# Kernel optimization log

Hardware: AMD Instinct MI355X
Metric: run time of the kernel (lower is better)

The kernel has to match this reference:

```python
import jax, jax.numpy as jnp
import numpy as np

C_IN = 256
C_INT = C_IN // 2  # inter_channels


def _conv1x1(x, w, b):
    # x: [B, Cin, H, W], w: [Cout, Cin], b: [Cout]
    return jnp.einsum('bchw,oc->bohw', x, w) + b[None, :, None, None]


def setup_inputs() -> dict:
    key = jax.random.key(0)
    ks = jax.random.split(key, 9)
    B, H, W = 8, 64, 64
    s_in = 1.0 / np.sqrt(C_IN)
    s_int = 1.0 / np.sqrt(C_INT)
    return {
        'x': jax.random.normal(ks[0], (B, C_IN, H, W), dtype=jnp.float32),
        'g_w': jax.random.normal(ks[1], (C_INT, C_IN), dtype=jnp.float32) * s_in,
        'g_b': jax.random.normal(ks[2], (C_INT,), dtype=jnp.float32) * s_in,
        'theta_w': jax.random.normal(ks[3], (C_INT, C_IN), dtype=jnp.float32) * s_in,
        'theta_b': jax.random.normal(ks[4], (C_INT,), dtype=jnp.float32) * s_in,
        'phi_w': jax.random.normal(ks[5], (C_INT, C_IN), dtype=jnp.float32) * s_in,
        'phi_b': jax.random.normal(ks[6], (C_INT,), dtype=jnp.float32) * s_in,
        'W_w': jax.random.normal(ks[7], (C_IN, C_INT), dtype=jnp.float32) * s_int,
        'W_b': jax.random.normal(ks[8], (C_IN,), dtype=jnp.float32) * s_int,
    }


def reference(x, g_w, g_b, theta_w, theta_b, phi_w, phi_b, W_w, W_b):
    B, C, H, W = x.shape
    N = H * W
    g_x = _conv1x1(x, g_w, g_b).reshape(B, C_INT, N)        # [B, Ci, N]
    theta_x = _conv1x1(x, theta_w, theta_b).reshape(B, C_INT, N)
    phi_x = _conv1x1(x, phi_w, phi_b).reshape(B, C_INT, N)
    # f[b, i, j] = theta[:, i] . phi[:, j]  (no scaling, per original)
    f = jnp.einsum('bci,bcj->bij', theta_x, phi_x)          # [B, N, N]
    f_div_C = jax.nn.softmax(f, axis=-1)
    y = jnp.einsum('bij,bcj->bci', f_div_C, g_x)            # [B, Ci, N]
    y = y.reshape(B, C_INT, H, W)
    y = _conv1x1(y, W_w, W_b)                               # [B, C, H, W]
    return x + y
```

## Files before the change

kernel.cpp:

```cpp
#include <hip/hip_runtime.h>

typedef _Float16 f16;
typedef _Float16 f16x4 __attribute__((ext_vector_type(4)));
typedef _Float16 f16x8 __attribute__((ext_vector_type(8)));
typedef __fp16 h2 __attribute__((ext_vector_type(2)));
typedef float f32x4 __attribute__((ext_vector_type(4)));
typedef float f32x16 __attribute__((ext_vector_type(16)));

#define MFMA16(a, b, c) __builtin_amdgcn_mfma_f32_16x16x32_f16(a, b, c, 0, 0, 0)
#define MFMA32(a, b, c) __builtin_amdgcn_mfma_f32_32x32x16_f16(a, b, c, 0, 0, 0)

#if defined(__has_builtin)
#if __has_builtin(__builtin_amdgcn_fdot2)
#define HAS_FDOT2 1
#endif
#endif

typedef const __attribute__((address_space(1))) void gvoid;
typedef __attribute__((address_space(3))) void lvoid;
#define GLDS16(g, l) __builtin_amdgcn_global_load_lds((gvoid*)(g), (lvoid*)(l), 16, 0, 0)

__global__ __launch_bounds__(256) void wcvt_k(
    const float* __restrict__ tw, const float* __restrict__ pw,
    const float* __restrict__ gw, const float* __restrict__ ww,
    f16* __restrict__ Wall, f16* __restrict__ Wepi) {
  int i = blockIdx.x * 256 + threadIdx.x;
  if (i < 384 * 256) {
    int c = i >> 8, cp = i & 255;
    float v = (c < 128) ? tw[c * 256 + cp]
            : (c < 256) ? pw[(c - 128) * 256 + cp]
                        : gw[(c - 256) * 256 + cp];
    Wall[i] = (f16)v;
  }
  int j = i - 384 * 256;
  if (j >= 0 && j < 256 * 128) Wepi[j] = (f16)ww[j];
}

__global__ __launch_bounds__(256) void proj_k(
    const float* __restrict__ x, const f16* __restrict__ Wall,
    const float* __restrict__ tb, const float* __restrict__ pb,
    const float* __restrict__ gb, f16* __restrict__ Q, f16* __restrict__ K,
    f16* __restrict__ Vt) {
  __shared__ f16 xs[64 * 264];
  __shared__ f16 vs[128 * 65];
  int b = blockIdx.x >> 6, nt = blockIdx.x & 63;
  int nbase = nt * 64;
  int tid = threadIdx.x;

  int nq = tid & 15, kq0 = tid >> 4;
#pragma unroll
  for (int p = 0; p < 4; ++p) {
    int kq = kq0 + 16 * p;
    float4 ld[4];
#pragma unroll
    for (int j = 0; j < 4; ++j)
      ld[j] = *(const float4*)(x + ((size_t)b * 256 + 4 * kq + j) * 4096 + nbase + 4 * nq);
#pragma unroll
    for (int e = 0; e < 4; ++e) {
      f16x4 wv = {(f16)((&ld[0].x)[e]), (f16)((&ld[1].x)[e]), (f16)((&ld[2].x)[e]),
                  (f16)((&ld[3].x)[e])};
      *(f16x4*)(&xs[(4 * nq + e) * 264 + 4 * kq]) = wv;
    }
  }
  __syncthreads();

  int w = tid >> 6, lane = tid & 63;
  int lr = lane & 15, lhi = lane >> 4;
  f16x8 a[8];
#pragma unroll
  for (int ks = 0; ks < 8; ++ks)
    a[ks] = *(const f16x8*)(&xs[(w * 16 + lr) * 264 + ks * 32 + lhi * 8]);
  f32x4 acc[24];
#pragma unroll
  for (int ct = 0; ct < 24; ++ct) {
    acc[ct] = {0.f, 0.f, 0.f, 0.f};
    const f16x8* wr = (const f16x8*)(Wall + (size_t)(ct * 16 + lr) * 256);
#pragma unroll
    for (int ks = 0; ks < 8; ++ks) acc[ct] = MFMA16(a[ks], wr[ks * 4 + lhi], acc[ct]);
  }
  int nloc = w * 16 + lhi * 4;
#pragma unroll
  for (int ct = 0; ct < 24; ++ct) {
    int c = ct * 16 + lr;
    float bias = (c < 128) ? tb[c] : (c < 256) ? pb[c - 128] : gb[c - 256];
#pragma unroll
    for (int r = 0; r < 4; ++r) {
      float v = acc[ct][r] + bias;
      int n = nbase + nloc + r;
      if (c < 128) {
        Q[((size_t)b * 4096 + n) * 128 + c] = (f16)v;
      } else if (c < 256) {
        int d = c - 128;
        int slot = ((d >> 4) << 6) + ((n & 31) << 1) + ((d >> 3) & 1);
        K[(size_t)b * 524288 + (size_t)(n >> 5) * 4096 + slot * 8 + (d & 7)] = (f16)v;
      } else {
        vs[(c - 256) * 65 + nloc + r] = (f16)v;
      }
    }
  }
  __syncthreads();
  f16* vo = Vt + (size_t)b * 524288;
  for (int rep = 0; rep < 32; ++rep) {
    int idx = rep * 256 + tid;
    int c = idx >> 6, j = idx & 63;
    int n = nbase + j;
    int nl = j & 31;
    int p = (nl & 3) | ((nl & 4) << 1) | ((nl & 8) >> 1) | (nl & 16);
    int g = p >> 3, e = p & 7;
    int slot = ((c >> 5) << 7) + ((g >> 1) << 6) + ((c & 31) << 1) + (g & 1);
    vo[(size_t)(n >> 5) * 4096 + slot * 8 + e] = vs[c * 65 + j];
  }
}

__global__ __launch_bounds__(256, 3) void attn_k(const f16* __restrict__ Q,
                                                 const f16* __restrict__ K,
                                                 const f16* __restrict__ Vt,
                                                 f16* __restrict__ Yp,
                                                 float2* __restrict__ ml) {
  __shared__ f16 Ks[2][32 * 128];
  __shared__ f16 Vs[2][128 * 32];
  const float L = 1.44269504f;
  int swzid = ((blockIdx.x & 7) << 7) | ((int)blockIdx.x >> 3);
  int b = swzid >> 7, rem = swzid & 127;
  int qt = rem >> 2, s = rem & 3;
  int qbase = qt * 128;
  int tile0 = s * 32;
  int tid = threadIdx.x;
  int w = tid >> 6, lane = tid & 63;
  int col = lane & 31, hi = lane >> 5;

  const f16* Qr = Q + ((size_t)b * 4096 + qbase + w * 32 + col) * 128;
  f16x8 bq[8];
#pragma unroll
  for (int ks = 0; ks < 8; ++ks) bq[ks] = *(const f16x8*)(Qr + ks * 16 + hi * 8);

  f32x16 yacc[4];
#pragma unroll
  for (int dt = 0; dt < 4; ++dt)
#pragma unroll
    for (int r = 0; r < 16; ++r) yacc[dt][r] = 0.f;
  float lv[4] = {0.f, 0.f, 0.f, 0.f};
  float m = -1e30f, nmL = 1e30f;

  const char* KbB = (const char*)(K + (size_t)b * 524288);
  const char* VbB = (const char*)(Vt + (size_t)b * 524288);
  char* KsB = (char*)&Ks[0][0];
  char* VsB = (char*)&Vs[0][0];

  auto stage = [&](int t, int buf) {
    size_t tb_ = (size_t)(tile0 + t) * 8192;
    const char* kb = KbB + tb_ + w * 2048 + lane * 16;
    const char* vb = VbB + tb_ + w * 2048 + lane * 16;
    char* kl = KsB + buf * 8192 + w * 2048;
    char* vl = VsB + buf * 8192 + w * 2048;
#pragma unroll
    for (int c = 0; c < 2; ++c) {
      GLDS16(kb + c * 1024, kl + c * 1024);
      GLDS16(vb + c * 1024, vl + c * 1024);
    }
  };

  int lanebase = col * 32 + hi * 16;

  stage(0, 0);

  for (int t = 0; t < 32; ++t) {
    int cur = t & 1;
    __syncthreads();
    if (t + 1 < 32) stage(t + 1, cur ^ 1);

    f32x16 s2;
#pragma unroll
    for (int r = 0; r < 16; ++r) s2[r] = 0.f;
    __builtin_amdgcn_s_setprio(1);
    {
      const char* kcur = KsB + cur * 8192 + lanebase;
#pragma unroll
      for (int ks = 0; ks < 8; ++ks) {
        f16x8 ak = *(const f16x8*)(kcur + ks * 1024);
        s2 = MFMA32(ak, bq[ks], s2);
      }
    }
    __builtin_amdgcn_s_setprio(0);

    float a0 = fmaxf(fmaxf(s2[0], s2[1]), s2[2]);
    float a1 = fmaxf(fmaxf(s2[3], s2[4]), s2[5]);
    float a2 = fmaxf(fmaxf(s2[6], s2[7]), s2[8]);
    float a3 = fmaxf(fmaxf(s2[9], s2[10]), s2[11]);
    float a4 = fmaxf(fmaxf(s2[12], s2[13]), s2[14]);
    float pm = fmaxf(fmaxf(fmaxf(a0, a1), fmaxf(a2, a3)), fmaxf(a4, s2[15]));
    pm = fmaxf(pm, __shfl_xor(pm, 32));
    if (pm > m + 8.f) {
      float sc = __expf(m - pm);
      m = pm;
      nmL = -m * L;
#pragma unroll
      for (int i = 0; i < 4; ++i) lv[i] *= sc;
#pragma unroll
      for (int dt = 0; dt < 4; ++dt)
#pragma unroll
        for (int r = 0; r < 16; ++r) yacc[dt][r] *= sc;
    }
#pragma unroll
    for (int r = 0; r < 16; ++r) s2[r] = exp2f(fmaf(s2[r], L, nmL));

    f16x8 pfrA, pfrB;
#pragma unroll
    for (int c = 0; c < 8; ++c) {
      pfrA[c] = (f16)s2[c];
      pfrB[c] = (f16)s2[8 + c];
    }
#if defined(HAS_FDOT2)
    {
      h2 one2 = {1.0f, 1.0f};
      const h2* pa = (const h2*)&pfrA;
      const h2* pb2 = (const h2*)&pfrB;
#pragma unroll
      for (int j = 0; j < 4; ++j) {
        lv[j] = __builtin_amdgcn_fdot2(pa[j], one2, lv[j], false);
        lv[j] = __builtin_amdgcn_fdot2(pb2[j], one2, lv[j], false);
      }
    }
#else
#pragma unroll
    for (int j = 0; j < 4; ++j)
      lv[j] += (float)pfrA[2 * j] + (float)pfrA[2 * j + 1] + (float)pfrB[2 * j] +
               (float)pfrB[2 * j + 1];
#endif

    __builtin_amdgcn_s_setprio(1);
    {
      const char* vcur = VsB + cur * 8192 + lanebase;
#pragma unroll
      for (int dt = 0; dt < 4; ++dt) {
        f16x8 av0 = *(const f16x8*)(vcur + dt * 2048);
        yacc[dt] = MFMA32(av0, pfrA, yacc[dt]);
        f16x8 av1 = *(const f16x8*)(vcur + dt * 2048 + 1024);
        yacc[dt] = MFMA32(av1, pfrB, yacc[dt]);
      }
    }
    __builtin_amdgcn_s_setprio(0);
  }

  float l = (lv[0] + lv[1]) + (lv[2] + lv[3]);
  l += __shfl_xor(l, 32);

  int rowG = b * 4096 + qbase + w * 32 + col;
  f16* yo = Yp + ((size_t)s * 32768 + rowG) * 128;
  float inv = 1.0f / l;
#pragma unroll
  for (int dt = 0; dt < 4; ++dt)
#pragma unroll
    for (int a = 0; a < 4; ++a) {
      f16x4 ov = {(f16)(yacc[dt][4 * a] * inv), (f16)(yacc[dt][4 * a + 1] * inv),
                  (f16)(yacc[dt][4 * a + 2] * inv), (f16)(yacc[dt][4 * a + 3] * inv)};
      *(f16x4*)(yo + dt * 32 + a * 8 + hi * 4) = ov;
    }
  if (hi == 0) ml[s * 32768 + rowG] = make_float2(m, l);
}

__global__ __launch_bounds__(256) void epi_k(const f16* __restrict__ Yp,
                                             const float2* __restrict__ ml,
                                             const f16* __restrict__ Wepi,
                                             const float* __restrict__ Wb,
                                             const float* __restrict__ x,
                                             float* __restrict__ out) {
  int b = blockIdx.x >> 6, nt = blockIdx.x & 63;
  int nbase = nt * 64;
  int w = threadIdx.x >> 6, lane = threadIdx.x & 63;
  int lr = lane & 15, lhi = lane >> 4;
  f16x8 by[4][4];
#pragma unroll
  for (int n4 = 0; n4 < 4; ++n4) {
    int row = b * 4096 + nbase + n4 * 16 + lr;
    float2 m0 = ml[row], m1 = ml[32768 + row], m2 = ml[65536 + row], m3 = ml[98304 + row];
    float mm = fmaxf(fmaxf(m0.x, m1.x), fmaxf(m2.x, m3.x));
    float w0 = m0.y * __expf(m0.x - mm), w1 = m1.y * __expf(m1.x - mm);
    float w2 = m2.y * __expf(m2.x - mm), w3 = m3.y * __expf(m3.x - mm);
    float inv = 1.f / (w0 + w1 + w2 + w3);
    w0 *= inv; w1 *= inv; w2 *= inv; w3 *= inv;
    size_t rb = (size_t)row * 128;
#pragma unroll
    for (int ks = 0; ks < 4; ++ks) {
      int eo = ks * 32 + lhi * 8;
      f16x8 a0 = *(const f16x8*)(Yp + rb + eo);
      f16x8 a1 = *(const f16x8*)(Yp + (size_t)32768 * 128 + rb + eo);
      f16x8 a2 = *(const f16x8*)(Yp + (size_t)65536 * 128 + rb + eo);
      f16x8 a3 = *(const f16x8*)(Yp + (size_t)98304 * 128 + rb + eo);
      f16x8 o;
#pragma unroll
      for (int e = 0; e < 8; ++e)
        o[e] = (f16)(w0 * (float)a0[e] + w1 * (float)a1[e] + w2 * (float)a2[e] +
                     w3 * (float)a3[e]);
      by[n4][ks] = o;
    }
  }
#pragma unroll
  for (int ot = 0; ot < 4; ++ot) {
    int o0 = w * 64 + ot * 16;
    const f16x8* wr = (const f16x8*)(Wepi + (size_t)(o0 + lr) * 128);
    f16x8 a[4];
#pragma unroll
    for (int ks = 0; ks < 4; ++ks) a[ks] = wr[ks * 4 + lhi];
#pragma unroll
    for (int n4 = 0; n4 < 4; ++n4) {
      f32x4 acc = {0.f, 0.f, 0.f, 0.f};
#pragma unroll
      for (int ks = 0; ks < 4; ++ks) acc = MFMA16(a[ks], by[n4][ks], acc);
#pragma unroll
      for (int r = 0; r < 4; ++r) {
        int o = o0 + lhi * 4 + r;
        int n = nbase + n4 * 16 + lr;
        size_t idx = ((size_t)b * 256 + o) * 4096 + n;
        out[idx] = x[idx] + Wb[o] + acc[r];
      }
    }
  }
}

extern "C" void kernel_launch(void* const* d_in, const int* in_sizes, int n_in,
                              void* d_out, int out_size, void* d_ws, size_t ws_size,
                              hipStream_t stream) {
  const float* x       = (const float*)d_in[0];
  const float* g_w     = (const float*)d_in[1];
  const float* g_b     = (const float*)d_in[2];
  const float* theta_w = (const float*)d_in[3];
  const float* theta_b = (const float*)d_in[4];
  const float* phi_w   = (const float*)d_in[5];
  const float* phi_b   = (const float*)d_in[6];
  const float* W_w     = (const float*)d_in[7];
  const float* W_b     = (const float*)d_in[8];
  float* out = (float*)d_out;

  f16* Q    = (f16*)d_ws;
  f16* Kk   = Q + (size_t)8 * 4096 * 128;
  f16* Vt   = Kk + (size_t)8 * 4096 * 128;
  f16* Wall = Vt + (size_t)8 * 4096 * 128;
  f16* Wepi = Wall + 384 * 256;
  float2* ml = (float2*)(Wepi + 256 * 128);
  f16* Yp   = (f16*)(ml + 4 * 32768);

  wcvt_k<<<512, 256, 0, stream>>>(theta_w, phi_w, g_w, W_w, Wall, Wepi);
  proj_k<<<512, 256, 0, stream>>>(x, Wall, theta_b, phi_b, g_b, Q, Kk, Vt);
  attn_k<<<1024, 256, 0, stream>>>(Q, Kk, Vt, Yp, ml);
  epi_k<<<512, 256, 0, stream>>>(Yp, ml, Wepi, W_b, x, out);
}
```

Measured before the change: 190.5 us.

## Double attention block to 512 threads sharing K/V tiles across 256 queries

```diff
diff --git a/kernel.cpp b/kernel.cpp
--- a/kernel.cpp
+++ b/kernel.cpp
@@ -112,7 +112,7 @@
   }
 }
 
-__global__ __launch_bounds__(256, 3) void attn_k(const f16* __restrict__ Q,
+__global__ __launch_bounds__(512, 4) void attn_k(const f16* __restrict__ Q,
                                                  const f16* __restrict__ K,
                                                  const f16* __restrict__ Vt,
                                                  f16* __restrict__ Yp,
@@ -120,10 +120,10 @@
   __shared__ f16 Ks[2][32 * 128];
   __shared__ f16 Vs[2][128 * 32];
   const float L = 1.44269504f;
-  int swzid = ((blockIdx.x & 7) << 7) | ((int)blockIdx.x >> 3);
-  int b = swzid >> 7, rem = swzid & 127;
+  int b = blockIdx.x & 7;
+  int rem = (int)blockIdx.x >> 3;
   int qt = rem >> 2, s = rem & 3;
-  int qbase = qt * 128;
+  int qbase = qt * 256;
   int tile0 = s * 32;
   int tid = threadIdx.x;
   int w = tid >> 6, lane = tid & 63;
@@ -139,7 +139,7 @@
   for (int dt = 0; dt < 4; ++dt)
 #pragma unroll
     for (int r = 0; r < 16; ++r) yacc[dt][r] = 0.f;
-  float lv[4] = {0.f, 0.f, 0.f, 0.f};
+  float lv[2] = {0.f, 0.f};
   float m = -1e30f, nmL = 1e30f;
 
   const char* KbB = (const char*)(K + (size_t)b * 524288);
@@ -148,16 +148,9 @@
   char* VsB = (char*)&Vs[0][0];
 
   auto stage = [&](int t, int buf) {
-    size_t tb_ = (size_t)(tile0 + t) * 8192;
-    const char* kb = KbB + tb_ + w * 2048 + lane * 16;
-    const char* vb = VbB + tb_ + w * 2048 + lane * 16;
-    char* kl = KsB + buf * 8192 + w * 2048;
-    char* vl = VsB + buf * 8192 + w * 2048;
-#pragma unroll
-    for (int c = 0; c < 2; ++c) {
-      GLDS16(kb + c * 1024, kl + c * 1024);
-      GLDS16(vb + c * 1024, vl + c * 1024);
-    }
+    size_t tb_ = (size_t)(tile0 + t) * 8192 + tid * 16;
+    GLDS16(KbB + tb_, KsB + buf * 8192 + tid * 16);
+    GLDS16(VbB + tb_, VsB + buf * 8192 + tid * 16);
   };
 
   int lanebase = col * 32 + hi * 16;
@@ -194,8 +187,8 @@
       float sc = __expf(m - pm);
       m = pm;
       nmL = -m * L;
-#pragma unroll
-      for (int i = 0; i < 4; ++i) lv[i] *= sc;
+      lv[0] *= sc;
+      lv[1] *= sc;
 #pragma unroll
       for (int dt = 0; dt < 4; ++dt)
 #pragma unroll
@@ -217,15 +210,16 @@
       const h2* pb2 = (const h2*)&pfrB;
 #pragma unroll
       for (int j = 0; j < 4; ++j) {
-        lv[j] = __builtin_amdgcn_fdot2(pa[j], one2, lv[j], false);
-        lv[j] = __builtin_amdgcn_fdot2(pb2[j], one2, lv[j], false);
+        lv[0] = __builtin_amdgcn_fdot2(pa[j], one2, lv[0], false);
+        lv[1] = __builtin_amdgcn_fdot2(pb2[j], one2, lv[1], false);
       }
     }
 #else
 #pragma unroll
-    for (int j = 0; j < 4; ++j)
-      lv[j] += (float)pfrA[2 * j] + (float)pfrA[2 * j + 1] + (float)pfrB[2 * j] +
-               (float)pfrB[2 * j + 1];
+    for (int j = 0; j < 4; ++j) {
+      lv[0] += (float)pfrA[2 * j] + (float)pfrA[2 * j + 1];
+      lv[1] += (float)pfrB[2 * j] + (float)pfrB[2 * j + 1];
+    }
 #endif
 
     __builtin_amdgcn_s_setprio(1);
@@ -242,7 +236,7 @@
     __builtin_amdgcn_s_setprio(0);
   }
 
-  float l = (lv[0] + lv[1]) + (lv[2] + lv[3]);
+  float l = lv[0] + lv[1];
   l += __shfl_xor(l, 32);
 
   int rowG = b * 4096 + qbase + w * 32 + col;
@@ -342,6 +336,6 @@
 
   wcvt_k<<<512, 256, 0, stream>>>(theta_w, phi_w, g_w, W_w, Wall, Wepi);
   proj_k<<<512, 256, 0, stream>>>(x, Wall, theta_b, phi_b, g_b, Q, Kk, Vt);
-  attn_k<<<1024, 256, 0, stream>>>(Q, Kk, Vt, Yp, ml);
+  attn_k<<<512, 512, 0, stream>>>(Q, Kk, Vt, Yp, ml);
   epi_k<<<512, 256, 0, stream>>>(Yp, ml, Wepi, W_b, x, out);
 }
```

Measured after the change: 193.4 us. No clear change (+1.5%).

## Software-pipeline attention with 4-stage LDS ring and halve KV split count

Applied to the files above, without the earlier changes.

```diff
diff --git a/kernel.cpp b/kernel.cpp
--- a/kernel.cpp
+++ b/kernel.cpp
@@ -112,19 +112,19 @@
   }
 }
 
-__global__ __launch_bounds__(256, 3) void attn_k(const f16* __restrict__ Q,
+__global__ __launch_bounds__(256, 2) void attn_k(const f16* __restrict__ Q,
                                                  const f16* __restrict__ K,
                                                  const f16* __restrict__ Vt,
                                                  f16* __restrict__ Yp,
                                                  float2* __restrict__ ml) {
-  __shared__ f16 Ks[2][32 * 128];
-  __shared__ f16 Vs[2][128 * 32];
+  __shared__ f16 Ks[4][32 * 128];
+  __shared__ f16 Vs[4][128 * 32];
   const float L = 1.44269504f;
-  int swzid = ((blockIdx.x & 7) << 7) | ((int)blockIdx.x >> 3);
-  int b = swzid >> 7, rem = swzid & 127;
-  int qt = rem >> 2, s = rem & 3;
+  int swzid = ((blockIdx.x & 7) << 6) | ((int)blockIdx.x >> 3);
+  int b = swzid >> 6, rem = swzid & 63;
+  int qt = rem >> 1, s = rem & 1;
   int qbase = qt * 128;
-  int tile0 = s * 32;
+  int tile0 = s * 64;
   int tid = threadIdx.x;
   int w = tid >> 6, lane = tid & 63;
   int col = lane & 31, hi = lane >> 5;
@@ -147,12 +147,12 @@
   char* KsB = (char*)&Ks[0][0];
   char* VsB = (char*)&Vs[0][0];
 
-  auto stage = [&](int t, int buf) {
+  auto stage = [&](int t) {
     size_t tb_ = (size_t)(tile0 + t) * 8192;
     const char* kb = KbB + tb_ + w * 2048 + lane * 16;
     const char* vb = VbB + tb_ + w * 2048 + lane * 16;
-    char* kl = KsB + buf * 8192 + w * 2048;
-    char* vl = VsB + buf * 8192 + w * 2048;
+    char* kl = KsB + (t & 3) * 8192 + w * 2048;
+    char* vl = VsB + (t & 3) * 8192 + w * 2048;
 #pragma unroll
     for (int c = 0; c < 2; ++c) {
       GLDS16(kb + c * 1024, kl + c * 1024);
@@ -162,33 +162,26 @@
 
   int lanebase = col * 32 + hi * 16;
 
-  stage(0, 0);
-
-  for (int t = 0; t < 32; ++t) {
-    int cur = t & 1;
-    __syncthreads();
-    if (t + 1 < 32) stage(t + 1, cur ^ 1);
-
-    f32x16 s2;
-#pragma unroll
-    for (int r = 0; r < 16; ++r) s2[r] = 0.f;
+  auto qkt = [&](int p, f32x16& sN) {
+    const char* kcur = KsB + (p & 3) * 8192 + lanebase;
+#pragma unroll
+    for (int r = 0; r < 16; ++r) sN[r] = 0.f;
     __builtin_amdgcn_s_setprio(1);
-    {
-      const char* kcur = KsB + cur * 8192 + lanebase;
-#pragma unroll
-      for (int ks = 0; ks < 8; ++ks) {
-        f16x8 ak = *(const f16x8*)(kcur + ks * 1024);
-        s2 = MFMA32(ak, bq[ks], s2);
-      }
+#pragma unroll
+    for (int ks = 0; ks < 8; ++ks) {
+      f16x8 ak = *(const f16x8*)(kcur + ks * 1024);
+      sN = MFMA32(ak, bq[ks], sN);
     }
     __builtin_amdgcn_s_setprio(0);
-
-    float a0 = fmaxf(fmaxf(s2[0], s2[1]), s2[2]);
-    float a1 = fmaxf(fmaxf(s2[3], s2[4]), s2[5]);
-    float a2 = fmaxf(fmaxf(s2[6], s2[7]), s2[8]);
-    float a3 = fmaxf(fmaxf(s2[9], s2[10]), s2[11]);
-    float a4 = fmaxf(fmaxf(s2[12], s2[13]), s2[14]);
-    float pm = fmaxf(fmaxf(fmaxf(a0, a1), fmaxf(a2, a3)), fmaxf(a4, s2[15]));
+  };
+
+  auto smpv = [&](int t, f32x16& sO) {
+    float a0 = fmaxf(fmaxf(sO[0], sO[1]), sO[2]);
+    float a1 = fmaxf(fmaxf(sO[3], sO[4]), sO[5]);
+    float a2 = fmaxf(fmaxf(sO[6], sO[7]), sO[8]);
+    float a3 = fmaxf(fmaxf(sO[9], sO[10]), sO[11]);
+    float a4 = fmaxf(fmaxf(sO[12], sO[13]), sO[14]);
+    float pm = fmaxf(fmaxf(fmaxf(a0, a1), fmaxf(a2, a3)), fmaxf(a4, sO[15]));
     pm = fmaxf(pm, __shfl_xor(pm, 32));
     if (pm > m + 8.f) {
       float sc = __expf(m - pm);
@@ -202,13 +195,13 @@
         for (int r = 0; r < 16; ++r) yacc[dt][r] *= sc;
     }
 #pragma unroll
-    for (int r = 0; r < 16; ++r) s2[r] = exp2f(fmaf(s2[r], L, nmL));
+    for (int r = 0; r < 16; ++r) sO[r] = exp2f(fmaf(sO[r], L, nmL));
 
     f16x8 pfrA, pfrB;
 #pragma unroll
     for (int c = 0; c < 8; ++c) {
-      pfrA[c] = (f16)s2[c];
-      pfrB[c] = (f16)s2[8 + c];
+      pfrA[c] = (f16)sO[c];
+      pfrB[c] = (f16)sO[8 + c];
     }
 #if defined(HAS_FDOT2)
     {
@@ -227,20 +220,54 @@
       lv[j] += (float)pfrA[2 * j] + (float)pfrA[2 * j + 1] + (float)pfrB[2 * j] +
                (float)pfrB[2 * j + 1];
 #endif
-
     __builtin_amdgcn_s_setprio(1);
-    {
-      const char* vcur = VsB + cur * 8192 + lanebase;
-#pragma unroll
-      for (int dt = 0; dt < 4; ++dt) {
-        f16x8 av0 = *(const f16x8*)(vcur + dt * 2048);
-        yacc[dt] = MFMA32(av0, pfrA, yacc[dt]);
-        f16x8 av1 = *(const f16x8*)(vcur + dt * 2048 + 1024);
-        yacc[dt] = MFMA32(av1, pfrB, yacc[dt]);
-      }
+    const char* vcur = VsB + (t & 3) * 8192 + lanebase;
+#pragma unroll
+    for (int dt = 0; dt < 4; ++dt) {
+      f16x8 av0 = *(const f16x8*)(vcur + dt * 2048);
+      yacc[dt] = MFMA32(av0, pfrA, yacc[dt]);
+      f16x8 av1 = *(const f16x8*)(vcur + dt * 2048 + 1024);
+      yacc[dt] = MFMA32(av1, pfrB, yacc[dt]);
     }
     __builtin_amdgcn_s_setprio(0);
-  }
+  };
+
+#define PH_WAIT4 asm volatile("s_waitcnt vmcnt(4)" ::: "memory")
+#define PH_WAIT0 asm volatile("s_waitcnt vmcnt(0)" ::: "memory")
+
+  f32x16 sA, sB;
+  stage(0);
+  stage(1);
+  PH_WAIT4;
+  __builtin_amdgcn_s_barrier();
+  stage(2);
+  qkt(0, sA);
+  PH_WAIT4;
+  __builtin_amdgcn_s_barrier();
+  stage(3);
+  qkt(1, sB);
+  smpv(0, sA);
+  for (int p = 2; p < 62; p += 2) {
+    PH_WAIT4;
+    __builtin_amdgcn_s_barrier();
+    stage(p + 2);
+    qkt(p, sA);
+    smpv(p - 1, sB);
+    PH_WAIT4;
+    __builtin_amdgcn_s_barrier();
+    stage(p + 3);
+    qkt(p + 1, sB);
+    smpv(p, sA);
+  }
+  PH_WAIT4;
+  __builtin_amdgcn_s_barrier();
+  qkt(62, sA);
+  smpv(61, sB);
+  PH_WAIT0;
+  __builtin_amdgcn_s_barrier();
+  qkt(63, sB);
+  smpv(62, sA);
+  smpv(63, sB);
 
   float l = (lv[0] + lv[1]) + (lv[2] + lv[3]);
   l += __shfl_xor(l, 32);
@@ -269,29 +296,26 @@
   int nbase = nt * 64;
   int w = threadIdx.x >> 6, lane = threadIdx.x & 63;
   int lr = lane & 15, lhi = lane >> 4;
+  const f16* yb1 = Yp + (size_t)32768 * 128;
   f16x8 by[4][4];
 #pragma unroll
   for (int n4 = 0; n4 < 4; ++n4) {
     int row = b * 4096 + nbase + n4 * 16 + lr;
-    float2 m0 = ml[row], m1 = ml[32768 + row], m2 = ml[65536 + row], m3 = ml[98304 + row];
-    float mm = fmaxf(fmaxf(m0.x, m1.x), fmaxf(m2.x, m3.x));
+    float2 m0 = ml[row], m1 = ml[32768 + row];
+    float mm = fmaxf(m0.x, m1.x);
     float w0 = m0.y * __expf(m0.x - mm), w1 = m1.y * __expf(m1.x - mm);
-    float w2 = m2.y * __expf(m2.x - mm), w3 = m3.y * __expf(m3.x - mm);
-    float inv = 1.f / (w0 + w1 + w2 + w3);
-    w0 *= inv; w1 *= inv; w2 *= inv; w3 *= inv;
+    float inv = 1.f / (w0 + w1);
+    w0 *= inv;
+    w1 *= inv;
     size_t rb = (size_t)row * 128;
 #pragma unroll
     for (int ks = 0; ks < 4; ++ks) {
       int eo = ks * 32 + lhi * 8;
       f16x8 a0 = *(const f16x8*)(Yp + rb + eo);
-      f16x8 a1 = *(const f16x8*)(Yp + (size_t)32768 * 128 + rb + eo);
-      f16x8 a2 = *(const f16x8*)(Yp + (size_t)65536 * 128 + rb + eo);
-      f16x8 a3 = *(const f16x8*)(Yp + (size_t)98304 * 128 + rb + eo);
+      f16x8 a1 = *(const f16x8*)(yb1 + rb + eo);
       f16x8 o;
 #pragma unroll
-      for (int e = 0; e < 8; ++e)
-        o[e] = (f16)(w0 * (float)a0[e] + w1 * (float)a1[e] + w2 * (float)a2[e] +
-                     w3 * (float)a3[e]);
+      for (int e = 0; e < 8; ++e) o[e] = (f16)(w0 * (float)a0[e] + w1 * (float)a1[e]);
       by[n4][ks] = o;
     }
   }
@@ -338,10 +362,10 @@
   f16* Wall = Vt + (size_t)8 * 4096 * 128;
   f16* Wepi = Wall + 384 * 256;
   float2* ml = (float2*)(Wepi + 256 * 128);
-  f16* Yp   = (f16*)(ml + 4 * 32768);
+  f16* Yp   = (f16*)(ml + 2 * 32768);
 
   wcvt_k<<<512, 256, 0, stream>>>(theta_w, phi_w, g_w, W_w, Wall, Wepi);
   proj_k<<<512, 256, 0, stream>>>(x, Wall, theta_b, phi_b, g_b, Q, Kk, Vt);
-  attn_k<<<1024, 256, 0, stream>>>(Q, Kk, Vt, Yp, ml);
+  attn_k<<<512, 256, 0, stream>>>(Q, Kk, Vt, Yp, ml);
   epi_k<<<512, 256, 0, stream>>>(Yp, ml, Wepi, W_b, x, out);
 }
```

After: 184.8 us, median of 2. 3.0% less time.

## Process two 32-row query tiles per wave in attention kernel to reuse K/V loads

Applied to the files above, without the earlier changes.

```diff
diff --git a/kernel.cpp b/kernel.cpp
--- a/kernel.cpp
+++ b/kernel.cpp
@@ -112,7 +112,7 @@
   }
 }
 
-__global__ __launch_bounds__(256, 3) void attn_k(const f16* __restrict__ Q,
+__global__ __launch_bounds__(256, 2) void attn_k(const f16* __restrict__ Q,
                                                  const f16* __restrict__ K,
                                                  const f16* __restrict__ Vt,
                                                  f16* __restrict__ Yp,
@@ -120,27 +120,34 @@
   __shared__ f16 Ks[2][32 * 128];
   __shared__ f16 Vs[2][128 * 32];
   const float L = 1.44269504f;
-  int swzid = ((blockIdx.x & 7) << 7) | ((int)blockIdx.x >> 3);
-  int b = swzid >> 7, rem = swzid & 127;
+  int swzid = ((blockIdx.x & 7) << 6) | ((int)blockIdx.x >> 3);
+  int b = swzid >> 6, rem = swzid & 63;
   int qt = rem >> 2, s = rem & 3;
-  int qbase = qt * 128;
+  int qbase = qt * 256;
   int tile0 = s * 32;
   int tid = threadIdx.x;
   int w = tid >> 6, lane = tid & 63;
   int col = lane & 31, hi = lane >> 5;
 
-  const f16* Qr = Q + ((size_t)b * 4096 + qbase + w * 32 + col) * 128;
-  f16x8 bq[8];
-#pragma unroll
-  for (int ks = 0; ks < 8; ++ks) bq[ks] = *(const f16x8*)(Qr + ks * 16 + hi * 8);
-
-  f32x16 yacc[4];
+  const f16* Qr = Q + ((size_t)b * 4096 + qbase + w * 64 + col) * 128;
+  f16x8 bq0[8], bq1[8];
+#pragma unroll
+  for (int ks = 0; ks < 8; ++ks) {
+    bq0[ks] = *(const f16x8*)(Qr + ks * 16 + hi * 8);
+    bq1[ks] = *(const f16x8*)(Qr + 32 * 128 + ks * 16 + hi * 8);
+  }
+
+  f32x16 y0[4], y1[4];
 #pragma unroll
   for (int dt = 0; dt < 4; ++dt)
 #pragma unroll
-    for (int r = 0; r < 16; ++r) yacc[dt][r] = 0.f;
-  float lv[4] = {0.f, 0.f, 0.f, 0.f};
-  float m = -1e30f, nmL = 1e30f;
+    for (int r = 0; r < 16; ++r) {
+      y0[dt][r] = 0.f;
+      y1[dt][r] = 0.f;
+    }
+  float lv0 = 0.f, lv1 = 0.f;
+  float m0 = -1e30f, nmL0 = 1e30f;
+  float m1 = -1e30f, nmL1 = 1e30f;
 
   const char* KbB = (const char*)(K + (size_t)b * 524288);
   const char* VbB = (const char*)(Vt + (size_t)b * 524288);
@@ -169,63 +176,106 @@
     __syncthreads();
     if (t + 1 < 32) stage(t + 1, cur ^ 1);
 
-    f32x16 s2;
-#pragma unroll
-    for (int r = 0; r < 16; ++r) s2[r] = 0.f;
+    f32x16 s0, s1;
+#pragma unroll
+    for (int r = 0; r < 16; ++r) {
+      s0[r] = 0.f;
+      s1[r] = 0.f;
+    }
     __builtin_amdgcn_s_setprio(1);
     {
       const char* kcur = KsB + cur * 8192 + lanebase;
 #pragma unroll
       for (int ks = 0; ks < 8; ++ks) {
         f16x8 ak = *(const f16x8*)(kcur + ks * 1024);
-        s2 = MFMA32(ak, bq[ks], s2);
+        s0 = MFMA32(ak, bq0[ks], s0);
+        s1 = MFMA32(ak, bq1[ks], s1);
       }
     }
     __builtin_amdgcn_s_setprio(0);
 
-    float a0 = fmaxf(fmaxf(s2[0], s2[1]), s2[2]);
-    float a1 = fmaxf(fmaxf(s2[3], s2[4]), s2[5]);
-    float a2 = fmaxf(fmaxf(s2[6], s2[7]), s2[8]);
-    float a3 = fmaxf(fmaxf(s2[9], s2[10]), s2[11]);
-    float a4 = fmaxf(fmaxf(s2[12], s2[13]), s2[14]);
-    float pm = fmaxf(fmaxf(fmaxf(a0, a1), fmaxf(a2, a3)), fmaxf(a4, s2[15]));
-    pm = fmaxf(pm, __shfl_xor(pm, 32));
-    if (pm > m + 8.f) {
-      float sc = __expf(m - pm);
-      m = pm;
-      nmL = -m * L;
-#pragma unroll
-      for (int i = 0; i < 4; ++i) lv[i] *= sc;
-#pragma unroll
-      for (int dt = 0; dt < 4; ++dt)
-#pragma unroll
-        for (int r = 0; r < 16; ++r) yacc[dt][r] *= sc;
-    }
-#pragma unroll
-    for (int r = 0; r < 16; ++r) s2[r] = exp2f(fmaf(s2[r], L, nmL));
-
-    f16x8 pfrA, pfrB;
-#pragma unroll
-    for (int c = 0; c < 8; ++c) {
-      pfrA[c] = (f16)s2[c];
-      pfrB[c] = (f16)s2[8 + c];
+    f16x8 p0A, p0B, p1A, p1B;
+    {
+      float a0 = fmaxf(fmaxf(s0[0], s0[1]), s0[2]);
+      float a1 = fmaxf(fmaxf(s0[3], s0[4]), s0[5]);
+      float a2 = fmaxf(fmaxf(s0[6], s0[7]), s0[8]);
+      float a3 = fmaxf(fmaxf(s0[9], s0[10]), s0[11]);
+      float a4 = fmaxf(fmaxf(s0[12], s0[13]), s0[14]);
+      float pm = fmaxf(fmaxf(fmaxf(a0, a1), fmaxf(a2, a3)), fmaxf(a4, s0[15]));
+      pm = fmaxf(pm, __shfl_xor(pm, 32));
+      if (pm > m0 + 8.f) {
+        float sc = __expf(m0 - pm);
+        m0 = pm;
+        nmL0 = -m0 * L;
+        lv0 *= sc;
+#pragma unroll
+        for (int dt = 0; dt < 4; ++dt)
+#pragma unroll
+          for (int r = 0; r < 16; ++r) y0[dt][r] *= sc;
+      }
+#pragma unroll
+      for (int r = 0; r < 16; ++r) s0[r] = exp2f(fmaf(s0[r], L, nmL0));
+#pragma unroll
+      for (int c = 0; c < 8; ++c) {
+        p0A[c] = (f16)s0[c];
+        p0B[c] = (f16)s0[8 + c];
+      }
+    }
+    {
+      float a0 = fmaxf(fmaxf(s1[0], s1[1]), s1[2]);
+      float a1 = fmaxf(fmaxf(s1[3], s1[4]), s1[5]);
+      float a2 = fmaxf(fmaxf(s1[6], s1[7]), s1[8]);
+      float a3 = fmaxf(fmaxf(s1[9], s1[10]), s1[11]);
+      float a4 = fmaxf(fmaxf(s1[12], s1[13]), s1[14]);
+      float pm = fmaxf(fmaxf(fmaxf(a0, a1), fmaxf(a2, a3)), fmaxf(a4, s1[15]));
+      pm = fmaxf(pm, __shfl_xor(pm, 32));
+      if (pm > m1 + 8.f) {
+        float sc = __expf(m1 - pm);
+        m1 = pm;
+        nmL1 = -m1 * L;
+        lv1 *= sc;
+#pragma unroll
+        for (int dt = 0; dt < 4; ++dt)
+#pragma unroll
+          for (int r = 0; r < 16; ++r) y1[dt][r] *= sc;
+      }
+#pragma unroll
+      for (int r = 0; r < 16; ++r) s1[r] = exp2f(fmaf(s1[r], L, nmL1));
+#pragma unroll
+      for (int c = 0; c < 8; ++c) {
+        p1A[c] = (f16)s1[c];
+        p1B[c] = (f16)s1[8 + c];
+      }
     }
 #if defined(HAS_FDOT2)
     {
       h2 one2 = {1.0f, 1.0f};
-      const h2* pa = (const h2*)&pfrA;
-      const h2* pb2 = (const h2*)&pfrB;
+      const h2* q0a = (const h2*)&p0A;
+      const h2* q0b = (const h2*)&p0B;
+      const h2* q1a = (const h2*)&p1A;
+      const h2* q1b = (const h2*)&p1B;
+      float t0 = 0.f, t1 = 0.f, t2 = 0.f, t3 = 0.f;
 #pragma unroll
       for (int j = 0; j < 4; ++j) {
-        lv[j] = __builtin_amdgcn_fdot2(pa[j], one2, lv[j], false);
-        lv[j] = __builtin_amdgcn_fdot2(pb2[j], one2, lv[j], false);
-      }
+        t0 = __builtin_amdgcn_fdot2(q0a[j], one2, t0, false);
+        t1 = __builtin_amdgcn_fdot2(q0b[j], one2, t1, false);
+        t2 = __builtin_amdgcn_fdot2(q1a[j], one2, t2, false);
+        t3 = __builtin_amdgcn_fdot2(q1b[j], one2, t3, false);
+      }
+      lv0 += t0 + t1;
+      lv1 += t2 + t3;
     }
 #else
-#pragma unroll
-    for (int j = 0; j < 4; ++j)
-      lv[j] += (float)pfrA[2 * j] + (float)pfrA[2 * j + 1] + (float)pfrB[2 * j] +
-               (float)pfrB[2 * j + 1];
+    {
+      float t0 = 0.f, t1 = 0.f;
+#pragma unroll
+      for (int c = 0; c < 8; ++c) {
+        t0 += (float)p0A[c] + (float)p0B[c];
+        t1 += (float)p1A[c] + (float)p1B[c];
+      }
+      lv0 += t0;
+      lv1 += t1;
+    }
 #endif
 
     __builtin_amdgcn_s_setprio(1);
@@ -234,29 +284,38 @@
 #pragma unroll
       for (int dt = 0; dt < 4; ++dt) {
         f16x8 av0 = *(const f16x8*)(vcur + dt * 2048);
-        yacc[dt] = MFMA32(av0, pfrA, yacc[dt]);
+        y0[dt] = MFMA32(av0, p0A, y0[dt]);
+        y1[dt] = MFMA32(av0, p1A, y1[dt]);
         f16x8 av1 = *(const f16x8*)(vcur + dt * 2048 + 1024);
-        yacc[dt] = MFMA32(av1, pfrB, yacc[dt]);
+        y0[dt] = MFMA32(av1, p0B, y0[dt]);
+        y1[dt] = MFMA32(av1, p1B, y1[dt]);
       }
     }
     __builtin_amdgcn_s_setprio(0);
   }
 
-  float l = (lv[0] + lv[1]) + (lv[2] + lv[3]);
-  l += __shfl_xor(l, 32);
-
-  int rowG = b * 4096 + qbase + w * 32 + col;
-  f16* yo = Yp + ((size_t)s * 32768 + rowG) * 128;
-  float inv = 1.0f / l;
+  float l0 = lv0 + __shfl_xor(lv0, 32);
+  float l1 = lv1 + __shfl_xor(lv1, 32);
+
+  int rowG = b * 4096 + qbase + w * 64 + col;
+  float inv0 = 1.0f / l0, inv1 = 1.0f / l1;
+  f16* yo0 = Yp + ((size_t)s * 32768 + rowG) * 128;
+  f16* yo1 = yo0 + (size_t)32 * 128;
 #pragma unroll
   for (int dt = 0; dt < 4; ++dt)
 #pragma unroll
     for (int a = 0; a < 4; ++a) {
-      f16x4 ov = {(f16)(yacc[dt][4 * a] * inv), (f16)(yacc[dt][4 * a + 1] * inv),
-                  (f16)(yacc[dt][4 * a + 2] * inv), (f16)(yacc[dt][4 * a + 3] * inv)};
-      *(f16x4*)(yo + dt * 32 + a * 8 + hi * 4) = ov;
-    }
-  if (hi == 0) ml[s * 32768 + rowG] = make_float2(m, l);
+      f16x4 ov0 = {(f16)(y0[dt][4 * a] * inv0), (f16)(y0[dt][4 * a + 1] * inv0),
+                   (f16)(y0[dt][4 * a + 2] * inv0), (f16)(y0[dt][4 * a + 3] * inv0)};
+      *(f16x4*)(yo0 + dt * 32 + a * 8 + hi * 4) = ov0;
+      f16x4 ov1 = {(f16)(y1[dt][4 * a] * inv1), (f16)(y1[dt][4 * a + 1] * inv1),
+                   (f16)(y1[dt][4 * a + 2] * inv1), (f16)(y1[dt][4 * a + 3] * inv1)};
+      *(f16x4*)(yo1 + dt * 32 + a * 8 + hi * 4) = ov1;
+    }
+  if (hi == 0) {
+    ml[s * 32768 + rowG] = make_float2(m0, l0);
+    ml[s * 32768 + rowG + 32] = make_float2(m1, l1);
+  }
 }
 
 __global__ __launch_bounds__(256) void epi_k(const f16* __restrict__ Yp,
@@ -342,6 +401,6 @@
 
   wcvt_k<<<512, 256, 0, stream>>>(theta_w, phi_w, g_w, W_w, Wall, Wepi);
   proj_k<<<512, 256, 0, stream>>>(x, Wall, theta_b, phi_b, g_b, Q, Kk, Vt);
-  attn_k<<<1024, 256, 0, stream>>>(Q, Kk, Vt, Yp, ml);
+  attn_k<<<512, 256, 0, stream>>>(Q, Kk, Vt, Yp, ml);
   epi_k<<<512, 256, 0, stream>>>(Yp, ml, Wepi, W_b, x, out);
 }
```

Measured after the change: 187.2 us. Within noise of the previous version (-1.7%).
